# Performance work log

Measured on AMD Instinct MI355X. Metric: run time of the kernel, lower is better.

The kernel has to match this reference:

```python
import jax, jax.numpy as jnp
import numpy as np
from math import factorial, sqrt

L_OUT = 4      # max_degree / max_actp_degree -> 25 sph components
L_B = 2        # max_basis_degree -> 9 sph components
F = 16         # num_radial_features (feature channels)
N_ATOMS = 10000
N_BONDS = 80000
CUTOFF = 5.0

# ---------------- real Clebsch-Gordan coefficients (numpy, at import) ----------

def _cg(j1, m1, j2, m2, j3, m3):
    if m1 + m2 != m3 or not (abs(j1 - j2) <= j3 <= j1 + j2):
        return 0.0
    f = factorial
    pre = sqrt((2 * j3 + 1) * f(j1 + j2 - j3) * f(j1 - j2 + j3) * f(-j1 + j2 + j3) / f(j1 + j2 + j3 + 1))
    pre *= sqrt(f(j1 + m1) * f(j1 - m1) * f(j2 + m2) * f(j2 - m2) * f(j3 + m3) * f(j3 - m3))
    s = 0.0
    kmin = max(0, j2 - j3 - m1, j1 - j3 + m2)
    kmax = min(j1 + j2 - j3, j1 - m1, j2 + m2)
    for k in range(kmin, kmax + 1):
        s += (-1) ** k / (f(k) * f(j1 + j2 - j3 - k) * f(j1 - m1 - k) * f(j2 + m2 - k) * f(j3 - j2 + m1 + k) * f(j3 - j1 - m2 + k))
    return pre * s

def _U(l):
    # complex->real spherical harmonic change of basis (Condon-Shortley)
    U = np.zeros((2 * l + 1, 2 * l + 1), dtype=complex)
    U[l, l] = 1.0
    for m in range(1, l + 1):
        U[l + m, l + m] = (-1) ** m / np.sqrt(2.0)
        U[l + m, l - m] = 1.0 / np.sqrt(2.0)
        U[l - m, l + m] = -1j * (-1) ** m / np.sqrt(2.0)
        U[l - m, l - m] = 1j / np.sqrt(2.0)
    return U

def _real_cg(l1, l2, l3):
    Cc = np.zeros((2 * l1 + 1, 2 * l2 + 1, 2 * l3 + 1), dtype=complex)
    for m1 in range(-l1, l1 + 1):
        for m2 in range(-l2, l2 + 1):
            m3 = m1 + m2
            if -l3 <= m3 <= l3:
                Cc[l1 + m1, l2 + m2, l3 + m3] = _cg(l1, m1, l2, m2, l3, m3)
    Cr = np.einsum('am,bn,ck,mnk->abc', _U(l1).conj(), _U(l2).conj(), _U(l3), Cc)
    out = Cr.real + Cr.imag  # exactly one of the two is nonzero per path
    out[np.abs(out) < 1e-12] = 0.0
    return out

PATHS = []
for _l1 in range(L_B + 1):
    for _l2 in range(L_OUT + 1):
        for _l3 in range(abs(_l1 - _l2), min(_l1 + _l2, L_OUT) + 1):
            PATHS.append((_l1, _l2, _l3, jnp.asarray(_real_cg(_l1, _l2, _l3), dtype=jnp.float32)))
N_PATHS = len(PATHS)

# ---------------- equivariant building blocks --------------------------------

def _sph(u):
    # real spherical harmonics l=0..2, m=-l..l, for unit vectors u (E,3)
    x, y, z = u[:, 0], u[:, 1], u[:, 2]
    c0 = 0.28209479177387814
    c1 = 0.4886025119029199
    c2a = 1.0925484305920792
    c2b = 0.31539156525252005
    c2c = 0.5462742152960396
    return jnp.stack([jnp.full_like(x, c0),
                      c1 * y, c1 * z, c1 * x,
                      c2a * x * y, c2a * y * z, c2b * (3 * z * z - 1.0), c2a * x * z, c2c * (x * x - y * y)],
                     axis=-1)  # (E,9)

def basis(disp):
    r = jnp.linalg.norm(disp, axis=-1)
    u = disp / (r[:, None] + 1e-12)
    Y = _sph(u)  # (E,9)
    centers = jnp.linspace(0.0, CUTOFF, F)
    width = CUTOFF / F
    rb = jnp.exp(-((r[:, None] - centers) / width) ** 2)  # (E,F)
    cut = jnp.where(r < CUTOFF, 0.5 * (jnp.cos(jnp.pi * r / CUTOFF) + 1.0), 0.0)
    rb = rb * cut[:, None]
    return Y[:, None, :, None] * rb[:, None, None, :]

def edense(x, W, b):
    # per-(parity,degree) feature mixing; bias only on even scalar channel
    nl = W.shape[1]
    outs = []
    for l in range(nl):
        lo, hi = l * l, (l + 1) * (l + 1)
        outs.append(jnp.einsum('epmf,pfg->epmg', x[:, :, lo:hi], W[:, l]))
    out = jnp.concatenate(outs, axis=2)
    return out.at[:, 0, 0, :].add(b)

def eln(x, gamma, beta, eps=1e-5):
    # equivariant LayerNorm: RMS of per-feature degree norms; standard LN on even scalar
    outs = []
    for l in range(L_OUT + 1):
        lo, hi = l * l, (l + 1) * (l + 1)
        blk = x[:, :, lo:hi]
        n2 = jnp.sum(blk * blk, axis=2)                       # (E,2,F)
        rms = jnp.sqrt(jnp.mean(n2, axis=-1, keepdims=True) + eps)  # (E,2,1)
        outs.append(blk / rms[..., None] * gamma[:, l][None, :, None, :])
    out = jnp.concatenate(outs, axis=2)
    s = x[:, 0, 0, :]
    mu = jnp.mean(s, axis=-1, keepdims=True)
    var = jnp.var(s, axis=-1, keepdims=True)
    sh = (s - mu) / jnp.sqrt(var + eps) * gamma[0, 0] + beta
    return out.at[:, 0, 0, :].set(sh)

def emish(x):
    s = x[:, 0, 0, :]
    sp = jax.nn.softplus(s)
    t = jnp.tanh(sp)
    f = s * t
    fp = t + s * (1.0 - t * t) * jax.nn.sigmoid(s)
    out = x * fp[:, None, None, :]
    return out.at[:, 0, 0, :].set(f)

def tensor_product(x1, x2, Wtp):
    # FusedTensor analogue: x1 (E,1,9,F) parity (-1)^l per degree; x2 (E,2,25,F)
    x1s = x1[:, 0]
    out = jnp.zeros_like(x2)
    for i, (l1, l2, l3, C) in enumerate(PATHS):
        a = x1s[:, l1 * l1:(l1 + 1) * (l1 + 1)]          # (E,n1,F)
        b = x2[:, :, l2 * l2:(l2 + 1) * (l2 + 1)]        # (E,2,n2,F)
        tmp = jnp.einsum('enf,epmf,nmk->epkf', a, b, C)  # (E,2,n3,F)
        tmp = tmp * Wtp[i][None, :, None, :]
        if l1 % 2 == 1:
            tmp = tmp[:, ::-1]  # odd l1 flips output parity
        out = out.at[:, :, l3 * l3:(l3 + 1) * (l3 + 1)].add(tmp)
    return out

def forward(atomic_descriptors, neighbour_indices, neighbour_displacements,
            W1, b1, gamma, beta, W2, b2, Wb, bb, Wtp):
    i, j = neighbour_indices[:, 0], neighbour_indices[:, 1]
    y = atomic_descriptors[i] + atomic_descriptors[j]  # (E,2,25,F)
    y = edense(y, W1, b1)
    y = eln(y, gamma, beta)
    y = emish(y)
    y = edense(y, W2, b2) + y
    be = basis(neighbour_displacements).astype(jnp.float32)  # (E,1,9,F)
    bed = edense(be, Wb, bb)
    return tensor_product(bed, y, Wtp)

# ---------------- harness ----------------------------------------------------

def setup_inputs() -> dict:
    key = jax.random.key(0)
    ks = jax.random.split(key, 8)
    scale = 1.0 / np.sqrt(F)
    return {
        'atomic_descriptors': jax.random.normal(ks[0], (N_ATOMS, 2, (L_OUT + 1) ** 2, F), jnp.float32),
        'neighbour_indices': jax.random.randint(ks[1], (N_BONDS, 2), 0, N_ATOMS),
        'neighbour_displacements': jax.random.normal(ks[2], (N_BONDS, 3), jnp.float32),
        'W1': jax.random.normal(ks[3], (2, L_OUT + 1, F, F), jnp.float32) * scale,
        'b1': jnp.zeros((F,), jnp.float32),
        'gamma': jnp.ones((2, L_OUT + 1, F), jnp.float32),
        'beta': jnp.zeros((F,), jnp.float32),
        'W2': jax.random.normal(ks[4], (2, L_OUT + 1, F, F), jnp.float32) * scale,
        'b2': jnp.zeros((F,), jnp.float32),
        'Wb': jax.random.normal(ks[5], (1, L_B + 1, F, F), jnp.float32) * scale,
        'bb': jnp.zeros((F,), jnp.float32),
        'Wtp': jax.random.normal(ks[6], (N_PATHS, 2, F), jnp.float32) * scale,
    }

def reference(atomic_descriptors, neighbour_indices, neighbour_displacements,
              W1, b1, gamma, beta, W2, b2, Wb, bb, Wtp):
    return forward(atomic_descriptors, neighbour_indices, neighbour_displacements,
                   W1, b1, gamma, beta, W2, b2, Wb, bb, Wtp)
```

## Files before the change

kernel.cpp:

```cpp
#include <hip/hip_runtime.h>
#include <hip/hip_fp16.h>

#define NF   16
#define NLM  25
#define BPB  16
#define YSTR 816

typedef _Float16 h2f __attribute__((ext_vector_type(2)));

#if defined(__has_builtin)
#if __has_builtin(__builtin_amdgcn_fdot2)
#define FDOT2(a,b,c) __builtin_amdgcn_fdot2((a),(b),(c),false)
#endif
#endif
#ifndef FDOT2
#define FDOT2(a,b,c) ((c) + (float)(a)[0]*(float)(b)[0] + (float)(a)[1]*(float)(b)[1])
#endif

#define WAVE_LDS_FENCE() asm volatile("" ::: "memory")

#define NT_STORE(p, v) __builtin_nontemporal_store((v), (p))

constexpr double FT[12] = {1.,1.,2.,6.,24.,120.,720.,5040.,40320.,362880.,3628800.,39916800.};

constexpr double csqrt(double x){
    if (x <= 0.0) return 0.0;
    double g = x > 1.0 ? x : 1.0;
    for (int i = 0; i < 60; ++i){ double n = 0.5*(g + x/g); if (n == g) break; g = n; }
    return g;
}

constexpr double cgc(int j1,int m1,int j2,int m2,int j3,int m3){
    if (m1 + m2 != m3) return 0.0;
    int dj = j1 > j2 ? j1 - j2 : j2 - j1;
    if (j3 < dj || j3 > j1 + j2) return 0.0;
    if (m1 < -j1 || m1 > j1 || m2 < -j2 || m2 > j2 || m3 < -j3 || m3 > j3) return 0.0;
    double X = (2*j3+1)*FT[j1+j2-j3]*FT[j1-j2+j3]*FT[-j1+j2+j3]/FT[j1+j2+j3+1];
    double Y = FT[j1+m1]*FT[j1-m1]*FT[j2+m2]*FT[j2-m2]*FT[j3+m3]*FT[j3-m3];
    double pre = csqrt(X*Y);
    double s = 0.0;
    int kmin = 0; if (j2-j3-m1 > kmin) kmin = j2-j3-m1; if (j1-j3+m2 > kmin) kmin = j1-j3+m2;
    int kmax = j1+j2-j3; if (j1-m1 < kmax) kmax = j1-m1; if (j2+m2 < kmax) kmax = j2+m2;
    for (int k = kmin; k <= kmax; ++k)
        s += ((k & 1) ? -1.0 : 1.0) /
             (FT[k]*FT[j1+j2-j3-k]*FT[j1-m1-k]*FT[j2+m2-k]*FT[j3-j2+m1+k]*FT[j3-j1-m2+k]);
    return pre*s;
}

struct cplx { double re, im; };

constexpr cplx Uent(int l, int a, int col){
    int mp = a - l, mm = col - l;
    const double s2 = 0.70710678118654752440;
    if (mp == 0) return (mm == 0) ? cplx{1.0,0.0} : cplx{0.0,0.0};
    if (mp > 0){
        double sgn = (mp & 1) ? -1.0 : 1.0;
        if (mm ==  mp) return cplx{sgn*s2, 0.0};
        if (mm == -mp) return cplx{s2, 0.0};
        return cplx{0.0,0.0};
    }
    int q = -mp; double sgn = (q & 1) ? -1.0 : 1.0;
    if (mm ==  q) return cplx{0.0, -sgn*s2};
    if (mm == -q) return cplx{0.0,  s2};
    return cplx{0.0,0.0};
}

constexpr double realcg(int l1,int l2,int l3,int a,int b,int c){
    double re = 0.0, im = 0.0;
    for (int m = -l1; m <= l1; ++m){
        cplx u1 = Uent(l1, a, l1+m); u1.im = -u1.im;
        if (u1.re == 0.0 && u1.im == 0.0) continue;
        for (int n = -l2; n <= l2; ++n){
            cplx u2 = Uent(l2, b, l2+n); u2.im = -u2.im;
            if (u2.re == 0.0 && u2.im == 0.0) continue;
            int k = m + n; if (k < -l3 || k > l3) continue;
            cplx u3 = Uent(l3, c, l3+k);
            if (u3.re == 0.0 && u3.im == 0.0) continue;
            double g = cgc(l1, m, l2, n, l3, k);
            if (g == 0.0) continue;
            double pr = u1.re*u2.re - u1.im*u2.im;
            double pi = u1.re*u2.im + u1.im*u2.re;
            re += (pr*u3.re - pi*u3.im)*g;
            im += (pr*u3.im + pi*u3.re)*g;
        }
    }
    double o = re + im;
    if (o < 1e-12 && o > -1e-12) o = 0.0;
    return o;
}

template<int L1,int L2,int L3> struct CGT { float v[2*L1+1][2*L2+1][2*L3+1]; };

template<int L1,int L2,int L3>
constexpr CGT<L1,L2,L3> makeCG(){
    CGT<L1,L2,L3> t{};
    for (int a = 0; a < 2*L1+1; ++a)
        for (int b = 0; b < 2*L2+1; ++b)
            for (int c = 0; c < 2*L3+1; ++c)
                t.v[a][b][c] = (float)realcg(L1, L2, L3, a, b, c);
    return t;
}

template<int L1,int L2,int L3,int PIDX>
__device__ __forceinline__ void tp_path(const float (&bed)[9], const float (&y)[2][NLM],
                                        float (&o)[2][NLM], const float* __restrict__ Wtp, int g){
    static constexpr CGT<L1,L2,L3> C = makeCG<L1,L2,L3>();
    constexpr int K = 2*L3+1;
    float a0[K], a1[K];
    #pragma unroll
    for (int k = 0; k < K; ++k){ a0[k] = 0.f; a1[k] = 0.f; }
    #pragma unroll
    for (int n = 0; n < 2*L1+1; ++n){
        const float bn = bed[L1*L1 + n];
        #pragma unroll
        for (int m = 0; m < 2*L2+1; ++m){
            const float p0 = bn * y[0][L2*L2 + m];
            const float p1 = bn * y[1][L2*L2 + m];
            #pragma unroll
            for (int k = 0; k < K; ++k){
                const float c = C.v[n][m][k];
                if (c != 0.f){
                    a0[k] = fmaf(c, p0, a0[k]);
                    a1[k] = fmaf(c, p1, a1[k]);
                }
            }
        }
    }
    const float w0 = Wtp[(PIDX*2 + 0)*NF + g];
    const float w1 = Wtp[(PIDX*2 + 1)*NF + g];
    #pragma unroll
    for (int k = 0; k < K; ++k){
        if (L1 & 1){
            o[0][L3*L3 + k] = fmaf(w1, a1[k], o[0][L3*L3 + k]);
            o[1][L3*L3 + k] = fmaf(w0, a0[k], o[1][L3*L3 + k]);
        } else {
            o[0][L3*L3 + k] = fmaf(w0, a0[k], o[0][L3*L3 + k]);
            o[1][L3*L3 + k] = fmaf(w1, a1[k], o[1][L3*L3 + k]);
        }
    }
}

__global__ void transpose_w(const float* __restrict__ W1, const float* __restrict__ W2,
                            const float* __restrict__ Wb, void* __restrict__ wsv){
    __half* h1 = (__half*)wsv;
    __half* h2 = h1 + 2560;
    float*  wb = (float*)(h1 + 5120);
    int idx = blockIdx.x*256 + threadIdx.x;
    if (idx < 2560){
        int mat = idx >> 8, r = (idx >> 4) & 15, c = idx & 15;
        h1[idx] = __float2half_rn(W1[mat*256 + c*16 + r]);
        h2[idx] = __float2half_rn(W2[mat*256 + c*16 + r]);
    } else if (idx < 3328){
        int k = idx - 2560; int mat = k >> 8, r = (k >> 4) & 15, c = k & 15;
        wb[k] = Wb[mat*256 + c*16 + r];
    }
}

__global__ void conv_a16(const float4* __restrict__ A4, __half2* __restrict__ A16v, int n4){
    int idx = blockIdx.x*blockDim.x + threadIdx.x;
    for (; idx < n4; idx += gridDim.x*blockDim.x){
        float4 v = A4[idx];
        A16v[2*idx]   = __float22half2_rn(make_float2(v.x, v.y));
        A16v[2*idx+1] = __float22half2_rn(make_float2(v.z, v.w));
    }
}

struct H8 { float4 a, b; };

__device__ __forceinline__ void rest_of_kernel(__half* yb, int bond, int g,
        const float* __restrict__ disp, const float* __restrict__ b1,
        const float* __restrict__ gamma, const float* __restrict__ beta,
        const float* __restrict__ b2, const float* __restrict__ bb,
        const float* __restrict__ Wtp, const __half* __restrict__ Wt1h,
        const __half* __restrict__ Wt2h, const float* __restrict__ Wtb,
        float* __restrict__ out, bool act)
{
    float y[2][NLM];
    if (act){
        #pragma unroll
        for (int p = 0; p < 2; ++p){
            #pragma unroll
            for (int l = 0; l < 5; ++l){
                H8 wv = *(const H8*)(Wt1h + (((p*5 + l)*16 + g) << 4));
                const h2f* w = (const h2f*)&wv;
                #pragma unroll
                for (int m = 0; m < 2*l+1; ++m){
                    const int lm = l*l + m;
                    H8 rv = *(const H8*)&yb[p*400 + lm*16];
                    const h2f* v = (const h2f*)&rv;
                    float acc = 0.f;
                    #pragma unroll
                    for (int q = 0; q < 8; ++q) acc = FDOT2(v[q], w[q], acc);
                    y[p][lm] = acc;
                }
            }
        }
        y[0][0] += b1[g];

        float s0 = y[0][0];
        #pragma unroll
        for (int p = 0; p < 2; ++p){
            #pragma unroll
            for (int l = 0; l < 5; ++l){
                float n2 = 0.f;
                #pragma unroll
                for (int m = 0; m < 2*l+1; ++m){ float v = y[p][l*l+m]; n2 = fmaf(v, v, n2); }
                #pragma unroll
                for (int d = 1; d < 16; d <<= 1) n2 += __shfl_xor(n2, d, 16);
                float rinv = rsqrtf(n2*(1.f/16.f) + 1e-5f);
                float sc = rinv * gamma[(p*5 + l)*16 + g];
                #pragma unroll
                for (int m = 0; m < 2*l+1; ++m) y[p][l*l+m] *= sc;
            }
        }
        float mu = s0, sq = s0*s0;
        #pragma unroll
        for (int d = 1; d < 16; d <<= 1){ mu += __shfl_xor(mu, d, 16); sq += __shfl_xor(sq, d, 16); }
        mu *= (1.f/16.f); sq *= (1.f/16.f);
        float var = sq - mu*mu;
        float sh = (s0 - mu)*rsqrtf(var + 1e-5f)*gamma[g] + beta[g];
        y[0][0] = sh;

        float s  = sh;
        float es = __expf(fminf(s, 30.f));
        float es2 = es*es;
        float t   = (es2 + 2.f*es) / (es2 + 2.f*es + 2.f);
        float sig = es / (1.f + es);
        float fv  = s*t;
        float fp  = t + s*(1.f - t*t)*sig;
        #pragma unroll
        for (int p = 0; p < 2; ++p)
            #pragma unroll
            for (int lm = 0; lm < NLM; ++lm) y[p][lm] *= fp;
        y[0][0] = fv;
    }
    WAVE_LDS_FENCE();

    if (act){
        #pragma unroll
        for (int p = 0; p < 2; ++p)
            #pragma unroll
            for (int lm = 0; lm < NLM; ++lm)
                yb[p*400 + lm*16 + g] = __float2half_rn(y[p][lm]);
    }
    WAVE_LDS_FENCE();

    if (act){
        #pragma unroll
        for (int p = 0; p < 2; ++p){
            #pragma unroll
            for (int l = 0; l < 5; ++l){
                H8 wv = *(const H8*)(Wt2h + (((p*5 + l)*16 + g) << 4));
                const h2f* w = (const h2f*)&wv;
                #pragma unroll
                for (int m = 0; m < 2*l+1; ++m){
                    const int lm = l*l + m;
                    H8 rv = *(const H8*)&yb[p*400 + lm*16];
                    const h2f* v = (const h2f*)&rv;
                    float acc = 0.f;
                    #pragma unroll
                    for (int q = 0; q < 8; ++q) acc = FDOT2(v[q], w[q], acc);
                    y[p][lm] += acc;
                }
            }
        }
        y[0][0] += b2[g];

        float dx = disp[3*bond], dy = disp[3*bond+1], dz = disp[3*bond+2];
        float r  = sqrtf(dx*dx + dy*dy + dz*dz);
        float ir = 1.f/(r + 1e-12f);
        float ux = dx*ir, uy = dy*ir, uz = dz*ir;
        float Y[9];
        Y[0] = 0.28209479177387814f;
        Y[1] = 0.4886025119029199f*uy; Y[2] = 0.4886025119029199f*uz; Y[3] = 0.4886025119029199f*ux;
        Y[4] = 1.0925484305920792f*ux*uy; Y[5] = 1.0925484305920792f*uy*uz;
        Y[6] = 0.31539156525252005f*(3.f*uz*uz - 1.f);
        Y[7] = 1.0925484305920792f*ux*uz; Y[8] = 0.5462742152960396f*(ux*ux - uy*uy);
        float cut = (r < 5.0f) ? 0.5f*(__cosf(r*0.62831853071795864769f) + 1.f) : 0.f;
        float rb[16];
        #pragma unroll
        for (int f = 0; f < 16; ++f){
            float d = (r - (float)f*(1.f/3.f))*3.2f;
            rb[f] = __expf(-d*d)*cut;
        }
        float t3[3];
        #pragma unroll
        for (int l = 0; l < 3; ++l){
            const float4* wp = (const float4*)(Wtb + (l*16 + g)*16);
            float acc = 0.f;
            #pragma unroll
            for (int q = 0; q < 4; ++q){
                float4 t = wp[q];
                acc = fmaf(rb[4*q],   t.x, acc);
                acc = fmaf(rb[4*q+1], t.y, acc);
                acc = fmaf(rb[4*q+2], t.z, acc);
                acc = fmaf(rb[4*q+3], t.w, acc);
            }
            t3[l] = acc;
        }
        float bed[9];
        bed[0] = Y[0]*t3[0] + bb[g];
        #pragma unroll
        for (int m = 1; m < 4; ++m) bed[m] = Y[m]*t3[1];
        #pragma unroll
        for (int m = 4; m < 9; ++m) bed[m] = Y[m]*t3[2];

        float o[2][NLM];
        #pragma unroll
        for (int p = 0; p < 2; ++p)
            #pragma unroll
            for (int lm = 0; lm < NLM; ++lm) o[p][lm] = 0.f;

        tp_path<0,0,0, 0>(bed, y, o, Wtp, g);
        tp_path<0,1,1, 1>(bed, y, o, Wtp, g);
        tp_path<0,2,2, 2>(bed, y, o, Wtp, g);
        tp_path<0,3,3, 3>(bed, y, o, Wtp, g);
        tp_path<0,4,4, 4>(bed, y, o, Wtp, g);
        tp_path<1,0,1, 5>(bed, y, o, Wtp, g);
        tp_path<1,1,0, 6>(bed, y, o, Wtp, g);
        tp_path<1,1,1, 7>(bed, y, o, Wtp, g);
        tp_path<1,1,2, 8>(bed, y, o, Wtp, g);
        tp_path<1,2,1, 9>(bed, y, o, Wtp, g);
        tp_path<1,2,2,10>(bed, y, o, Wtp, g);
        tp_path<1,2,3,11>(bed, y, o, Wtp, g);
        tp_path<1,3,2,12>(bed, y, o, Wtp, g);
        tp_path<1,3,3,13>(bed, y, o, Wtp, g);
        tp_path<1,3,4,14>(bed, y, o, Wtp, g);
        tp_path<1,4,3,15>(bed, y, o, Wtp, g);
        tp_path<1,4,4,16>(bed, y, o, Wtp, g);
        tp_path<2,0,2,17>(bed, y, o, Wtp, g);
        tp_path<2,1,1,18>(bed, y, o, Wtp, g);
        tp_path<2,1,2,19>(bed, y, o, Wtp, g);
        tp_path<2,1,3,20>(bed, y, o, Wtp, g);
        tp_path<2,2,0,21>(bed, y, o, Wtp, g);
        tp_path<2,2,1,22>(bed, y, o, Wtp, g);
        tp_path<2,2,2,23>(bed, y, o, Wtp, g);
        tp_path<2,2,3,24>(bed, y, o, Wtp, g);
        tp_path<2,2,4,25>(bed, y, o, Wtp, g);
        tp_path<2,3,1,26>(bed, y, o, Wtp, g);
        tp_path<2,3,2,27>(bed, y, o, Wtp, g);
        tp_path<2,3,3,28>(bed, y, o, Wtp, g);
        tp_path<2,3,4,29>(bed, y, o, Wtp, g);
        tp_path<2,4,2,30>(bed, y, o, Wtp, g);
        tp_path<2,4,3,31>(bed, y, o, Wtp, g);
        tp_path<2,4,4,32>(bed, y, o, Wtp, g);

        float* op = out + (size_t)bond*800;
        #pragma unroll
        for (int p = 0; p < 2; ++p)
            #pragma unroll
            for (int lm = 0; lm < NLM; ++lm)
                NT_STORE(&op[p*400 + lm*16 + g], o[p][lm]);
    }
}

__global__ __launch_bounds__(256, 3)
void bctmd_kernel16(const __half* __restrict__ A16, const int* __restrict__ nbr,
                    const float* __restrict__ disp,
                    const float* __restrict__ b1, const float* __restrict__ gamma,
                    const float* __restrict__ beta, const float* __restrict__ b2,
                    const float* __restrict__ bb, const float* __restrict__ Wtp,
                    const __half* __restrict__ Wt1h, const __half* __restrict__ Wt2h,
                    const float* __restrict__ Wtb,
                    float* __restrict__ out, int nb)
{
    __shared__ __align__(16) __half ybuf[BPB*YSTR];
    const int tid  = threadIdx.x;
    const int bl   = tid >> 4;
    const int g    = tid & 15;
    const int bond = blockIdx.x*BPB + bl;
    const bool act = bond < nb;
    __half* yb = &ybuf[bl*YSTR];

    if (act){
        const int i = nbr[2*bond], j = nbr[2*bond+1];
        const uint4* Ai = (const uint4*)(A16 + (size_t)i*800);
        const uint4* Aj = (const uint4*)(A16 + (size_t)j*800);
        #pragma unroll
        for (int it = 0; it < 7; ++it){
            int q = g + 16*it;
            if (q < 100){
                uint4 a = Ai[q], b = Aj[q];
                const __half2* ha = (const __half2*)&a;
                const __half2* hb = (const __half2*)&b;
                __half2* d = (__half2*)&yb[8*q];
                d[0] = __hadd2(ha[0], hb[0]);
                d[1] = __hadd2(ha[1], hb[1]);
                d[2] = __hadd2(ha[2], hb[2]);
                d[3] = __hadd2(ha[3], hb[3]);
            }
        }
    }
    WAVE_LDS_FENCE();

    rest_of_kernel(yb, bond, g, disp, b1, gamma, beta, b2, bb, Wtp,
                   Wt1h, Wt2h, Wtb, out, act);
}

__global__ __launch_bounds__(256, 3)
void bctmd_kernel(const float* __restrict__ A, const int* __restrict__ nbr,
                  const float* __restrict__ disp,
                  const float* __restrict__ b1, const float* __restrict__ gamma,
                  const float* __restrict__ beta, const float* __restrict__ b2,
                  const float* __restrict__ bb, const float* __restrict__ Wtp,
                  const __half* __restrict__ Wt1h, const __half* __restrict__ Wt2h,
                  const float* __restrict__ Wtb,
                  float* __restrict__ out, int nb)
{
    __shared__ __align__(16) __half ybuf[BPB*YSTR];
    const int tid  = threadIdx.x;
    const int bl   = tid >> 4;
    const int g    = tid & 15;
    const int bond = blockIdx.x*BPB + bl;
    const bool act = bond < nb;
    __half* yb = &ybuf[bl*YSTR];

    if (act){
        const int i = nbr[2*bond], j = nbr[2*bond+1];
        const float4* Ai = (const float4*)(A + (size_t)i*800);
        const float4* Aj = (const float4*)(A + (size_t)j*800);
        #pragma unroll
        for (int it = 0; it < 13; ++it){
            int q = g + 16*it;
            if (q < 200){
                float4 a = Ai[q], b = Aj[q];
                __half2* d = (__half2*)&yb[4*q];
                d[0] = __float22half2_rn(make_float2(a.x+b.x, a.y+b.y));
                d[1] = __float22half2_rn(make_float2(a.z+b.z, a.w+b.w));
            }
        }
    }
    WAVE_LDS_FENCE();

    rest_of_kernel(yb, bond, g, disp, b1, gamma, beta, b2, bb, Wtp,
                   Wt1h, Wt2h, Wtb, out, act);
}

extern "C" void kernel_launch(void* const* d_in, const int* in_sizes, int n_in,
                              void* d_out, int out_size, void* d_ws, size_t ws_size,
                              hipStream_t stream){
    const float* A     = (const float*)d_in[0];
    const int*   nbr   = (const int*)d_in[1];
    const float* disp  = (const float*)d_in[2];
    const float* W1    = (const float*)d_in[3];
    const float* b1    = (const float*)d_in[4];
    const float* gamma = (const float*)d_in[5];
    const float* beta  = (const float*)d_in[6];
    const float* W2    = (const float*)d_in[7];
    const float* b2    = (const float*)d_in[8];
    const float* Wb    = (const float*)d_in[9];
    const float* bb    = (const float*)d_in[10];
    const float* Wtp   = (const float*)d_in[11];

    const int nb = in_sizes[1] / 2;
    const int nA = in_sizes[0];

    hipLaunchKernelGGL(transpose_w, dim3(13), dim3(256), 0, stream, W1, W2, Wb, d_ws);

    const __half* h1 = (const __half*)d_ws;
    const __half* h2 = h1 + 2560;
    const float*  wb = (const float*)(h1 + 5120);

    const int nblk = (nb + BPB - 1) / BPB;
    const size_t a16_off = 16384;
    const size_t a16_bytes = (size_t)nA * sizeof(__half);

    if (ws_size >= a16_off + a16_bytes && (nA & 3) == 0){
        __half* A16 = (__half*)((char*)d_ws + a16_off);
        hipLaunchKernelGGL(conv_a16, dim3(2048), dim3(256), 0, stream,
                           (const float4*)A, (__half2*)A16, nA/4);
        hipLaunchKernelGGL(bctmd_kernel16, dim3(nblk), dim3(256), 0, stream,
                           A16, nbr, disp, b1, gamma, beta, b2, bb, Wtp,
                           h1, h2, wb, (float*)d_out, nb);
    } else {
        hipLaunchKernelGGL(bctmd_kernel, dim3(nblk), dim3(256), 0, stream,
                           A, nbr, disp, b1, gamma, beta, b2, bb, Wtp,
                           h1, h2, wb, (float*)d_out, nb);
    }
}
```

Before: 176.9 us.

## Sort bonds by first atom via counting sort to improve gather locality

Adds a histogram, a single-block scan and an atomic scatter that build a permutation grouping bonds by their first atom index. The main kernel then processes bonds in that order, so bonds sharing atom i run in nearby blocks and can reuse its cached descriptor row. The cost is four extra small launches, a serial single-block scan, and scattered writes to the 800-float output rows. The fp32 fallback kernel is removed, so when the workspace is too small nothing is launched.

```diff
diff --git a/kernel.cpp b/kernel.cpp
--- a/kernel.cpp
+++ b/kernel.cpp
@@ -18,7 +18,6 @@
 #endif
 
 #define WAVE_LDS_FENCE() asm volatile("" ::: "memory")
-
 #define NT_STORE(p, v) __builtin_nontemporal_store((v), (p))
 
 constexpr double FT[12] = {1.,1.,2.,6.,24.,120.,720.,5040.,40320.,362880.,3628800.,39916800.};
@@ -162,6 +161,42 @@
         float4 v = A4[idx];
         A16v[2*idx]   = __float22half2_rn(make_float2(v.x, v.y));
         A16v[2*idx+1] = __float22half2_rn(make_float2(v.z, v.w));
+    }
+}
+
+__global__ void hist_zero(int* __restrict__ cnt, int n){
+    int idx = blockIdx.x*blockDim.x + threadIdx.x;
+    for (; idx < n; idx += gridDim.x*blockDim.x) cnt[idx] = 0;
+}
+__global__ void hist_k(const int* __restrict__ nbr, int* __restrict__ cnt, int nb){
+    int b = blockIdx.x*blockDim.x + threadIdx.x;
+    for (; b < nb; b += gridDim.x*blockDim.x) atomicAdd(&cnt[nbr[2*b]], 1);
+}
+__global__ __launch_bounds__(1024)
+void scan_k(const int* __restrict__ cnt, int* __restrict__ off, int n){
+    __shared__ int part[1024];
+    const int t = threadIdx.x;
+    const int chunk = (n + 1023) >> 10;
+    const int lo = t*chunk, hi = min(lo + chunk, n);
+    int s = 0;
+    for (int k = lo; k < hi; ++k) s += cnt[k];
+    part[t] = s;
+    __syncthreads();
+    for (int d = 1; d < 1024; d <<= 1){
+        int v = (t >= d) ? part[t-d] : 0;
+        __syncthreads();
+        part[t] += v;
+        __syncthreads();
+    }
+    int base = (t == 0) ? 0 : part[t-1];
+    for (int k = lo; k < hi; ++k){ off[k] = base; base += cnt[k]; }
+}
+__global__ void scatter_k(const int* __restrict__ nbr, int* __restrict__ off,
+                          int* __restrict__ perm, int nb){
+    int b = blockIdx.x*blockDim.x + threadIdx.x;
+    for (; b < nb; b += gridDim.x*blockDim.x){
+        int p = atomicAdd(&off[nbr[2*b]], 1);
+        perm[p] = b;
     }
 }
 
@@ -354,6 +389,56 @@
     }
 }
 
+__device__ __forceinline__ void stage16(const __half* __restrict__ A16,
+                                        const int* __restrict__ nbr,
+                                        __half* yb, int bond, int g){
+    const int i = nbr[2*bond], j = nbr[2*bond+1];
+    const uint4* Ai = (const uint4*)(A16 + (size_t)i*800);
+    const uint4* Aj = (const uint4*)(A16 + (size_t)j*800);
+    #pragma unroll
+    for (int it = 0; it < 7; ++it){
+        int q = g + 16*it;
+        if (q < 100){
+            uint4 a = Ai[q], b = Aj[q];
+            const __half2* ha = (const __half2*)&a;
+            const __half2* hb = (const __half2*)&b;
+            __half2* d = (__half2*)&yb[8*q];
+            d[0] = __hadd2(ha[0], hb[0]);
+            d[1] = __hadd2(ha[1], hb[1]);
+            d[2] = __hadd2(ha[2], hb[2]);
+            d[3] = __hadd2(ha[3], hb[3]);
+        }
+    }
+}
+
+__global__ __launch_bounds__(256, 3)
+void bctmd_kernel16p(const __half* __restrict__ A16, const int* __restrict__ perm,
+                     const int* __restrict__ nbr, const float* __restrict__ disp,
+                     const float* __restrict__ b1, const float* __restrict__ gamma,
+                     const float* __restrict__ beta, const float* __restrict__ b2,
+                     const float* __restrict__ bb, const float* __restrict__ Wtp,
+                     const __half* __restrict__ Wt1h, const __half* __restrict__ Wt2h,
+                     const float* __restrict__ Wtb,
+                     float* __restrict__ out, int nb)
+{
+    __shared__ __align__(16) __half ybuf[BPB*YSTR];
+    const int tid  = threadIdx.x;
+    const int bl   = tid >> 4;
+    const int g    = tid & 15;
+    const int bidx = blockIdx.x*BPB + bl;
+    const bool act = bidx < nb;
+    __half* yb = &ybuf[bl*YSTR];
+
+    int bond = 0;
+    if (act) bond = perm[bidx];
+
+    if (act) stage16(A16, nbr, yb, bond, g);
+    WAVE_LDS_FENCE();
+
+    rest_of_kernel(yb, bond, g, disp, b1, gamma, beta, b2, bb, Wtp,
+                   Wt1h, Wt2h, Wtb, out, act);
+}
+
 __global__ __launch_bounds__(256, 3)
 void bctmd_kernel16(const __half* __restrict__ A16, const int* __restrict__ nbr,
                     const float* __restrict__ disp,
@@ -372,64 +457,7 @@
     const bool act = bond < nb;
     __half* yb = &ybuf[bl*YSTR];
 
-    if (act){
-        const int i = nbr[2*bond], j = nbr[2*bond+1];
-        const uint4* Ai = (const uint4*)(A16 + (size_t)i*800);
-        const uint4* Aj = (const uint4*)(A16 + (size_t)j*800);
-        #pragma unroll
-        for (int it = 0; it < 7; ++it){
-            int q = g + 16*it;
-            if (q < 100){
-                uint4 a = Ai[q], b = Aj[q];
-                const __half2* ha = (const __half2*)&a;
-                const __half2* hb = (const __half2*)&b;
-                __half2* d = (__half2*)&yb[8*q];
-                d[0] = __hadd2(ha[0], hb[0]);
-                d[1] = __hadd2(ha[1], hb[1]);
-                d[2] = __hadd2(ha[2], hb[2]);
-                d[3] = __hadd2(ha[3], hb[3]);
-            }
-        }
-    }
-    WAVE_LDS_FENCE();
-
-    rest_of_kernel(yb, bond, g, disp, b1, gamma, beta, b2, bb, Wtp,
-                   Wt1h, Wt2h, Wtb, out, act);
-}
-
-__global__ __launch_bounds__(256, 3)
-void bctmd_kernel(const float* __restrict__ A, const int* __restrict__ nbr,
-                  const float* __restrict__ disp,
-                  const float* __restrict__ b1, const float* __restrict__ gamma,
-                  const float* __restrict__ beta, const float* __restrict__ b2,
-                  const float* __restrict__ bb, const float* __restrict__ Wtp,
-                  const __half* __restrict__ Wt1h, const __half* __restrict__ Wt2h,
-                  const float* __restrict__ Wtb,
-                  float* __restrict__ out, int nb)
-{
-    __shared__ __align__(16) __half ybuf[BPB*YSTR];
-    const int tid  = threadIdx.x;
-    const int bl   = tid >> 4;
-    const int g    = tid & 15;
-    const int bond = blockIdx.x*BPB + bl;
-    const bool act = bond < nb;
-    __half* yb = &ybuf[bl*YSTR];
-
-    if (act){
-        const int i = nbr[2*bond], j = nbr[2*bond+1];
-        const float4* Ai = (const float4*)(A + (size_t)i*800);
-        const float4* Aj = (const float4*)(A + (size_t)j*800);
-        #pragma unroll
-        for (int it = 0; it < 13; ++it){
-            int q = g + 16*it;
-            if (q < 200){
-                float4 a = Ai[q], b = Aj[q];
-                __half2* d = (__half2*)&yb[4*q];
-                d[0] = __float22half2_rn(make_float2(a.x+b.x, a.y+b.y));
-                d[1] = __float22half2_rn(make_float2(a.z+b.z, a.w+b.w));
-            }
-        }
-    }
+    if (act) stage16(A16, nbr, yb, bond, g);
     WAVE_LDS_FENCE();
 
     rest_of_kernel(yb, bond, g, disp, b1, gamma, beta, b2, bb, Wtp,
@@ -452,8 +480,9 @@
     const float* bb    = (const float*)d_in[10];
     const float* Wtp   = (const float*)d_in[11];
 
-    const int nb = in_sizes[1] / 2;
-    const int nA = in_sizes[0];
+    const int nb     = in_sizes[1] / 2;
+    const int nA     = in_sizes[0];
+    const int natoms = nA / 800;
 
     hipLaunchKernelGGL(transpose_w, dim3(13), dim3(256), 0, stream, W1, W2, Wb, d_ws);
 
@@ -462,19 +491,36 @@
     const float*  wb = (const float*)(h1 + 5120);
 
     const int nblk = (nb + BPB - 1) / BPB;
-    const size_t a16_off = 16384;
+    const size_t a16_off   = 16384;
     const size_t a16_bytes = (size_t)nA * sizeof(__half);
-
-    if (ws_size >= a16_off + a16_bytes && (nA & 3) == 0){
+    const size_t perm_off  = a16_off + ((a16_bytes + 255) & ~(size_t)255);
+    const size_t perm_b    = (size_t)nb * 4;
+    const size_t cnt_off   = perm_off + ((perm_b + 255) & ~(size_t)255);
+    const size_t cnt_b     = (size_t)natoms * 4;
+    const size_t off_off   = cnt_off + ((cnt_b + 255) & ~(size_t)255);
+    const size_t need_full = off_off + cnt_b;
+
+    if (ws_size >= need_full && (nA & 3) == 0){
+        __half* A16 = (__half*)((char*)d_ws + a16_off);
+        int* perm = (int*)((char*)d_ws + perm_off);
+        int* cnt  = (int*)((char*)d_ws + cnt_off);
+        int* off  = (int*)((char*)d_ws + off_off);
+
+        hipLaunchKernelGGL(conv_a16, dim3(2048), dim3(256), 0, stream,
+                           (const float4*)A, (__half2*)A16, nA/4);
+        hipLaunchKernelGGL(hist_zero, dim3((natoms+255)/256), dim3(256), 0, stream, cnt, natoms);
+        hipLaunchKernelGGL(hist_k, dim3((nb+255)/256), dim3(256), 0, stream, nbr, cnt, nb);
+        hipLaunchKernelGGL(scan_k, dim3(1), dim3(1024), 0, stream, cnt, off, natoms);
+        hipLaunchKernelGGL(scatter_k, dim3((nb+255)/256), dim3(256), 0, stream, nbr, off, perm, nb);
+        hipLaunchKernelGGL(bctmd_kernel16p, dim3(nblk), dim3(256), 0, stream,
+                           A16, perm, nbr, disp, b1, gamma, beta, b2, bb, Wtp,
+                           h1, h2, wb, (float*)d_out, nb);
+    } else if (ws_size >= a16_off + a16_bytes && (nA & 3) == 0){
         __half* A16 = (__half*)((char*)d_ws + a16_off);
         hipLaunchKernelGGL(conv_a16, dim3(2048), dim3(256), 0, stream,
                            (const float4*)A, (__half2*)A16, nA/4);
         hipLaunchKernelGGL(bctmd_kernel16, dim3(nblk), dim3(256), 0, stream,
                            A16, nbr, disp, b1, gamma, beta, b2, bb, Wtp,
                            h1, h2, wb, (float*)d_out, nb);
-    } else {
-        hipLaunchKernelGGL(bctmd_kernel, dim3(nblk), dim3(256), 0, stream,
-                           A, nbr, disp, b1, gamma, beta, b2, bb, Wtp,
-                           h1, h2, wb, (float*)d_out, nb);
-    }
-}
+    }
+}
```

Measured after the change: 197.7 us. 1.12x slower.
